# Performance work log

Hardware: AMD Instinct MI355X
Metric: run time of the kernel (lower is better)

The kernel has to match this reference:

```python
import jax, jax.numpy as jnp
import numpy as np

N, D_IN = 65536, 512
H1, H2, D_SH = 1024, 1024, 512   # shared net: num_nodes_shared = [1024, 1024, 512]
HI = 512                          # indiv hidden width, num_nodes_indiv = [512, 512]


def setup_inputs() -> dict:
    key = jax.random.key(0)
    ks = jax.random.split(key, 16)
    s = 0.02
    inp = {
        "input": jax.random.normal(ks[0], (N, D_IN), jnp.float32),
        "treatment": jax.random.randint(ks[1], (N,), 0, 2, jnp.int32),
        # shared net (hidden ReLU layers + linear output, all with bias)
        "W0": jax.random.normal(ks[2], (D_IN, H1), jnp.float32) * s,
        "b0": jnp.zeros((H1,), jnp.float32),
        "W1": jax.random.normal(ks[3], (H1, H2), jnp.float32) * s,
        "b1": jnp.zeros((H2,), jnp.float32),
        "W2": jax.random.normal(ks[4], (H2, D_SH), jnp.float32) * s,
        "b2": jnp.zeros((D_SH,), jnp.float32),
        # risk net 0 (output layer has no bias)
        "A0": jax.random.normal(ks[5], (D_SH, HI), jnp.float32) * s,
        "a0": jnp.zeros((HI,), jnp.float32),
        "A1": jax.random.normal(ks[6], (HI, HI), jnp.float32) * s,
        "a1": jnp.zeros((HI,), jnp.float32),
        "A2": jax.random.normal(ks[7], (HI, 1), jnp.float32) * s,
        # risk net 1
        "C0": jax.random.normal(ks[8], (D_SH, HI), jnp.float32) * s,
        "c0": jnp.zeros((HI,), jnp.float32),
        "C1": jax.random.normal(ks[9], (HI, HI), jnp.float32) * s,
        "c1": jnp.zeros((HI,), jnp.float32),
        "C2": jax.random.normal(ks[10], (HI, 1), jnp.float32) * s,
    }
    return inp


def _risk_net(h, U0, u0, U1, u1, U2):
    h = jax.nn.relu(h @ U0 + u0)
    h = jax.nn.relu(h @ U1 + u1)
    return h @ U2  # [N, 1], no output bias


def reference(input, treatment, W0, b0, W1, b1, W2, b2,
              A0, a0, A1, a1, A2, C0, c0, C1, c1, C2):
    # shared MLP
    h = jax.nn.relu(input @ W0 + b0)
    h = jax.nn.relu(h @ W1 + b1)
    out = h @ W2 + b2                     # [N, D_SH]
    # Binary expert routing. The torch code gathers samples per treatment,
    # runs each group through its own MLP and scatters results back; the
    # math is equivalent to applying both experts and selecting per sample.
    y0 = _risk_net(out, A0, a0, A1, a1, A2)[:, 0]  # [N]
    y1 = _risk_net(out, C0, c0, C1, c1, C2)[:, 0]  # [N]
    y = jnp.where(treatment == 0, y0, y1)          # [N]
    return (y, out)
```

## Files before the change

kernel.cpp:

```cpp
#include <hip/hip_runtime.h>
#include <hip/hip_bf16.h>
#include <stdint.h>

typedef short short8 __attribute__((ext_vector_type(8)));
typedef float f32x4 __attribute__((ext_vector_type(4)));

#define NSAMP 65536
#define AS1 __attribute__((address_space(1)))
#define AS3 __attribute__((address_space(3)))

__device__ __forceinline__ unsigned f2bf(float f) {
    union { float f; unsigned u; } v; v.f = f;
    unsigned u = v.u;
    u += 0x7fffu + ((u >> 16) & 1u);
    return u >> 16;
}


__global__ void k_convert_bf16(const float* __restrict__ in, unsigned short* __restrict__ out, int n8) {
    int i = blockIdx.x * blockDim.x + threadIdx.x;
    if (i >= n8) return;
    const float4* p = (const float4*)in + (size_t)i * 2;
    float4 a = p[0], b = p[1];
    short8 o;
    o[0] = (short)f2bf(a.x); o[1] = (short)f2bf(a.y);
    o[2] = (short)f2bf(a.z); o[3] = (short)f2bf(a.w);
    o[4] = (short)f2bf(b.x); o[5] = (short)f2bf(b.y);
    o[6] = (short)f2bf(b.z); o[7] = (short)f2bf(b.w);
    ((short8*)out)[i] = o;
}

struct PrepArgs {
    const float *W0, *W1, *W2, *A0, *C0, *A1, *C1, *a0v, *c0v;
    unsigned short *W0T, *W1T, *W2T, *RT0, *A1T, *C1T;
    float *bcat, *yout;
};
__global__ void k_prep(PrepArgs p) {
    int i = blockIdx.x * blockDim.x + threadIdx.x;
    if (i < 524288)  { int k = i >> 10, n = i & 1023; p.W0T[n * 512 + k] = f2bf(p.W0[i]); return; }
    i -= 524288;
    if (i < 1048576) { int k = i >> 10, n = i & 1023; p.W1T[n * 1024 + k] = f2bf(p.W1[i]); return; }
    i -= 1048576;
    if (i < 524288)  { int k = i >> 9, n = i & 511; p.W2T[n * 1024 + k] = f2bf(p.W2[i]); return; }
    i -= 524288;
    if (i < 262144)  { int k = i >> 9, n = i & 511; p.RT0[n * 512 + k] = f2bf(p.A0[i]); return; }
    i -= 262144;
    if (i < 262144)  { int k = i >> 9, n = i & 511; p.RT0[(512 + n) * 512 + k] = f2bf(p.C0[i]); return; }
    i -= 262144;
    if (i < 262144)  { int k = i >> 9, n = i & 511; p.A1T[n * 512 + k] = f2bf(p.A1[i]); return; }
    i -= 262144;
    if (i < 262144)  { int k = i >> 9, n = i & 511; p.C1T[n * 512 + k] = f2bf(p.C1[i]); return; }
    i -= 262144;
    if (i < 512)     { p.bcat[i] = p.a0v[i]; return; }
    i -= 512;
    if (i < 512)     { p.bcat[512 + i] = p.c0v[i]; return; }
    i -= 512;
    if (i < 65536)   { p.yout[i] = 0.f; return; }
}

template<int MODE>
__global__ __launch_bounds__(512, 2)
void k_gemm256(const unsigned short* __restrict__ A, int lda,
               const unsigned short* __restrict__ BT, const unsigned short* __restrict__ BT2,
               const float* __restrict__ bias, const float* __restrict__ bias2,
               unsigned short* __restrict__ Cbf, float* __restrict__ Cf32,
               const float* __restrict__ w2, const float* __restrict__ w2b,
               const int* __restrict__ TRt, float* __restrict__ ydot,
               int Ncols, int K, int TPB)
{
    __shared__ __align__(16) char lds[131072];

    const int tid  = threadIdx.x;
    const int lane = tid & 63;
    const int wid  = tid >> 6;
    const int wr   = wid >> 2;
    const int wcn  = wid & 3;

    const int bid = (int)((blockIdx.x & 7) * 32 + (blockIdx.x >> 3));
    const int cls = bid % TPB;
    const int w   = bid / TPB;
    const int MSTEP = 256 / TPB;

    int n0e, cOff = 0, expert = 0;
    const unsigned short* Bsel = BT;
    if (MODE == 2) {
        expert = cls >> 1;
        n0e = (cls & 1) << 8;
        cOff = expert << 9;
        if (expert) Bsel = BT2;
    } else {
        n0e = cls << 8;
    }

    const int srow = tid >> 2;
    const int scs  = (tid & 3) ^ ((srow >> 1) & 3);
    const int ldst = wid * 1024;

    const unsigned short* gB0 = Bsel + (size_t)(n0e + srow) * K + scs * 8;
    const unsigned short* gB1 = gB0 + (size_t)128 * K;
    const size_t dA = (size_t)MSTEP * 256 * lda;
    const unsigned short* cA0 = A + (size_t)((w << 8) + srow) * lda + cOff + scs * 8;
    const unsigned short* cA1 = cA0 + (size_t)128 * lda;

#define STAGE_BLK(dbuf, blkoff, g0, g1, koff)                                            \
    do {                                                                                 \
        __builtin_amdgcn_global_load_lds((const AS1 void*)((g0) + (koff)),               \
                                         (AS3 void*)((dbuf) + (blkoff) + ldst), 16, 0, 0); \
        __builtin_amdgcn_global_load_lds((const AS1 void*)((g1) + (koff)),               \
                                         (AS3 void*)((dbuf) + (blkoff) + 8192 + ldst), 16, 0, 0); \
    } while (0)

    int aOff[8], bOff[4];
#pragma unroll
    for (int i = 0; i < 8; ++i) {
        int r = wr * 128 + i * 16 + (lane & 15);
        aOff[i] = r * 64 + ((((lane >> 4) ^ ((r >> 1) & 3))) << 4);
    }
#pragma unroll
    for (int j = 0; j < 4; ++j) {
        int r = wcn * 64 + j * 16 + (lane & 15);
        bOff[j] = r * 64 + ((((lane >> 4) ^ ((r >> 1) & 3))) << 4);
    }

    f32x4 acc[8][4];
#pragma unroll
    for (int i = 0; i < 8; ++i)
#pragma unroll
        for (int j = 0; j < 4; ++j) acc[i][j] = (f32x4)0.f;

    const int KT  = K >> 6;
    const int TOT = TPB * KT;

    STAGE_BLK(lds, 0,     cA0, cA1, 0);
    STAGE_BLK(lds, 32768, gB0, gB1, 0);
    STAGE_BLK(lds, 16384, cA0, cA1, 32);
    STAGE_BLK(lds, 49152, gB0, gB1, 32);
    asm volatile("s_waitcnt vmcnt(4)" ::: "memory");
    __builtin_amdgcn_s_barrier();

    int g = 0;
    for (int tau = 0; tau < TPB; ++tau) {
        const unsigned short* nA0 = cA0 + dA;
        const unsigned short* nA1 = cA1 + dA;

        for (int t = 0; t < KT; ++t, ++g) {
            const char* sbuf = lds + (g & 1) * 65536;
            char* dbuf = lds + ((g + 1) & 1) * 65536;
            const bool inTile = (t + 1 < KT);
            const bool st = (g + 1 < TOT);
            const unsigned short* sA0 = inTile ? cA0 : nA0;
            const unsigned short* sA1 = inTile ? cA1 : nA1;
            const int koff = inTile ? ((t + 1) << 6) : 0;
            short8 af[4], bfv[4];

#pragma unroll
            for (int i = 0; i < 4; ++i) af[i]  = *(const short8*)(sbuf + aOff[i]);
#pragma unroll
            for (int j = 0; j < 4; ++j) bfv[j] = *(const short8*)(sbuf + 32768 + bOff[j]);
            if (st) STAGE_BLK(dbuf, 0, sA0, sA1, koff);
            __builtin_amdgcn_s_barrier();
            asm volatile("s_waitcnt lgkmcnt(0)" ::: "memory");
            __builtin_amdgcn_sched_barrier(0);
            __builtin_amdgcn_s_setprio(1);
#pragma unroll
            for (int i = 0; i < 4; ++i)
#pragma unroll
                for (int j = 0; j < 4; ++j)
                    acc[i][j] = __builtin_amdgcn_mfma_f32_16x16x32_bf16(bfv[j], af[i], acc[i][j], 0, 0, 0);
            __builtin_amdgcn_s_setprio(0);
            __builtin_amdgcn_s_barrier();

#pragma unroll
            for (int i = 0; i < 4; ++i) af[i] = *(const short8*)(sbuf + aOff[4 + i]);
            if (st) STAGE_BLK(dbuf, 32768, gB0, gB1, koff);
            __builtin_amdgcn_s_barrier();
            asm volatile("s_waitcnt lgkmcnt(0)" ::: "memory");
            __builtin_amdgcn_sched_barrier(0);
            __builtin_amdgcn_s_setprio(1);
#pragma unroll
            for (int i = 0; i < 4; ++i)
#pragma unroll
                for (int j = 0; j < 4; ++j)
                    acc[4 + i][j] = __builtin_amdgcn_mfma_f32_16x16x32_bf16(bfv[j], af[i], acc[4 + i][j], 0, 0, 0);
            __builtin_amdgcn_s_setprio(0);
            if (st) { asm volatile("s_waitcnt vmcnt(4)" ::: "memory"); }
            else    { asm volatile("s_waitcnt vmcnt(0)" ::: "memory"); }
            __builtin_amdgcn_sched_barrier(0);
            __builtin_amdgcn_s_barrier();

#pragma unroll
            for (int i = 0; i < 4; ++i) af[i]  = *(const short8*)(sbuf + 16384 + aOff[i]);
#pragma unroll
            for (int j = 0; j < 4; ++j) bfv[j] = *(const short8*)(sbuf + 49152 + bOff[j]);
            if (st) STAGE_BLK(dbuf, 16384, sA0, sA1, koff + 32);
            __builtin_amdgcn_s_barrier();
            asm volatile("s_waitcnt lgkmcnt(0)" ::: "memory");
            __builtin_amdgcn_sched_barrier(0);
            __builtin_amdgcn_s_setprio(1);
#pragma unroll
            for (int i = 0; i < 4; ++i)
#pragma unroll
                for (int j = 0; j < 4; ++j)
                    acc[i][j] = __builtin_amdgcn_mfma_f32_16x16x32_bf16(bfv[j], af[i], acc[i][j], 0, 0, 0);
            __builtin_amdgcn_s_setprio(0);
            __builtin_amdgcn_s_barrier();

#pragma unroll
            for (int i = 0; i < 4; ++i) af[i] = *(const short8*)(sbuf + 16384 + aOff[4 + i]);
            if (st) STAGE_BLK(dbuf, 49152, gB0, gB1, koff + 32);
            __builtin_amdgcn_s_barrier();
            asm volatile("s_waitcnt lgkmcnt(0)" ::: "memory");
            __builtin_amdgcn_sched_barrier(0);
            __builtin_amdgcn_s_setprio(1);
#pragma unroll
            for (int i = 0; i < 4; ++i)
#pragma unroll
                for (int j = 0; j < 4; ++j)
                    acc[4 + i][j] = __builtin_amdgcn_mfma_f32_16x16x32_bf16(bfv[j], af[i], acc[4 + i][j], 0, 0, 0);
            __builtin_amdgcn_s_setprio(0);
            if (st) { asm volatile("s_waitcnt vmcnt(4)" ::: "memory"); }
            __builtin_amdgcn_sched_barrier(0);
            __builtin_amdgcn_s_barrier();
        }

        const int m0 = (w + MSTEP * tau) << 8;
        if (MODE == 2) {
            const float* be = expert ? bias2 : bias;
            const float* we = expert ? w2b : w2;
            const int nb = n0e + wcn * 64 + ((lane >> 4) << 2);
            f32x4 bv[4], wv[4];
#pragma unroll
            for (int j = 0; j < 4; ++j) {
                bv[j] = *(const f32x4*)(be + nb + j * 16);
                wv[j] = *(const f32x4*)(we + nb + j * 16);
            }
#pragma unroll
            for (int i = 0; i < 8; ++i) {
                float p = 0.f;
#pragma unroll
                for (int j = 0; j < 4; ++j)
#pragma unroll
                    for (int r = 0; r < 4; ++r)
                        p += fmaxf(acc[i][j][r] + bv[j][r], 0.f) * wv[j][r];
                p += __shfl_xor(p, 16);
                p += __shfl_xor(p, 32);
                const int m = m0 + wr * 128 + i * 16 + (lane & 15);
                if (lane < 16 && TRt[m] == expert) atomicAdd(&ydot[m], p);
            }
        } else {
            const int nb = n0e + wcn * 64 + ((lane >> 4) << 2);
            f32x4 bv[4];
#pragma unroll
            for (int j = 0; j < 4; ++j) bv[j] = *(const f32x4*)(bias + nb + j * 16);
#pragma unroll
            for (int i = 0; i < 8; ++i) {
                const int m = m0 + wr * 128 + i * 16 + (lane & 15);
                unsigned short* pb = Cbf + (size_t)m * Ncols + nb;
#pragma unroll
                for (int j = 0; j < 4; ++j) {
                    f32x4 v = acc[i][j] + bv[j];
                    if (MODE == 0) {
#pragma unroll
                        for (int r = 0; r < 4; ++r) v[r] = fmaxf(v[r], 0.f);
                    }
                    if (MODE == 1) *(f32x4*)(Cf32 + (size_t)m * Ncols + nb + j * 16) = v;
                    unsigned long long pk =
                        (unsigned long long)(f2bf(v[0]) | (f2bf(v[1]) << 16)) |
                        ((unsigned long long)(f2bf(v[2]) | (f2bf(v[3]) << 16)) << 32);
                    *(unsigned long long*)(pb + j * 16) = pk;
                }
            }
        }

#pragma unroll
        for (int i = 0; i < 8; ++i)
#pragma unroll
            for (int j = 0; j < 4; ++j) acc[i][j] = (f32x4)0.f;
        cA0 = nA0; cA1 = nA1;
    }
#undef STAGE_BLK
}


extern "C" void kernel_launch(void* const* d_in, const int* in_sizes, int n_in,
                              void* d_out, int out_size, void* d_ws, size_t ws_size,
                              hipStream_t stream) {
    const float* X  = (const float*)d_in[0];
    const int*  TR  = (const int*)d_in[1];
    const float* W0 = (const float*)d_in[2];  const float* b0 = (const float*)d_in[3];
    const float* W1 = (const float*)d_in[4];  const float* b1 = (const float*)d_in[5];
    const float* W2 = (const float*)d_in[6];  const float* b2 = (const float*)d_in[7];
    const float* A0 = (const float*)d_in[8];  const float* a0 = (const float*)d_in[9];
    const float* A1 = (const float*)d_in[10]; const float* a1 = (const float*)d_in[11];
    const float* A2 = (const float*)d_in[12];
    const float* C0 = (const float*)d_in[13]; const float* c0 = (const float*)d_in[14];
    const float* C1 = (const float*)d_in[15]; const float* c1 = (const float*)d_in[16];
    const float* C2 = (const float*)d_in[17];

    float* y_out   = (float*)d_out;
    float* out_out = (float*)d_out + NSAMP;

    char* ws = (char*)d_ws;
    size_t off = 0;
    auto alloc = [&](size_t bytes) -> char* {
        char* p = ws + off;
        off += (bytes + 255) & ~(size_t)255;
        return p;
    };
    unsigned short* Xb  = (unsigned short*)alloc((size_t)NSAMP * 512 * 2);
    unsigned short* H1b = (unsigned short*)alloc((size_t)NSAMP * 1024 * 2);
    unsigned short* H2b = (unsigned short*)alloc((size_t)NSAMP * 1024 * 2);
    unsigned short* OUTb = H1b;
    unsigned short* R01  = H2b;
    unsigned short* W0T = (unsigned short*)alloc(512 * 1024 * 2);
    unsigned short* W1T = (unsigned short*)alloc(1024 * 1024 * 2);
    unsigned short* W2T = (unsigned short*)alloc(1024 * 512 * 2);
    unsigned short* RT0 = (unsigned short*)alloc(1024 * 512 * 2);
    unsigned short* A1T = (unsigned short*)alloc(512 * 512 * 2);
    unsigned short* C1T = (unsigned short*)alloc(512 * 512 * 2);
    float* bcat = (float*)alloc(1024 * 4);

    k_convert_bf16<<<(NSAMP * 512 / 8 + 255) / 256, 256, 0, stream>>>(X, Xb, NSAMP * 512 / 8);
    PrepArgs pa;
    pa.W0 = W0; pa.W1 = W1; pa.W2 = W2; pa.A0 = A0; pa.C0 = C0; pa.A1 = A1; pa.C1 = C1;
    pa.a0v = a0; pa.c0v = c0;
    pa.W0T = W0T; pa.W1T = W1T; pa.W2T = W2T; pa.RT0 = RT0; pa.A1T = A1T; pa.C1T = C1T;
    pa.bcat = bcat; pa.yout = y_out;
    k_prep<<<(3212288 + 255) / 256, 256, 0, stream>>>(pa);

    k_gemm256<0><<<256, 512, 0, stream>>>(Xb, 512, W0T, nullptr, b0, nullptr,
                                          H1b, nullptr, nullptr, nullptr, nullptr, nullptr,
                                          1024, 512, 4);
    k_gemm256<0><<<256, 512, 0, stream>>>(H1b, 1024, W1T, nullptr, b1, nullptr,
                                          H2b, nullptr, nullptr, nullptr, nullptr, nullptr,
                                          1024, 1024, 4);
    k_gemm256<1><<<256, 512, 0, stream>>>(H2b, 1024, W2T, nullptr, b2, nullptr,
                                          OUTb, out_out, nullptr, nullptr, nullptr, nullptr,
                                          512, 1024, 2);

    k_gemm256<0><<<256, 512, 0, stream>>>(OUTb, 512, RT0, nullptr, bcat, nullptr,
                                          R01, nullptr, nullptr, nullptr, nullptr, nullptr,
                                          1024, 512, 4);

    k_gemm256<2><<<256, 512, 0, stream>>>(R01, 1024, A1T, C1T, a1, c1,
                                          nullptr, nullptr, A2, C2, TR, y_out,
                                          512, 512, 4);
}
```

Before: 575.3 us.

## Prefetch LDS fragments across K-steps and cut per-step barriers in GEMM main loop

```diff
diff --git a/kernel.cpp b/kernel.cpp
--- a/kernel.cpp
+++ b/kernel.cpp
@@ -137,6 +137,13 @@
     STAGE_BLK(lds, 49152, gB0, gB1, 32);
     asm volatile("s_waitcnt vmcnt(4)" ::: "memory");
     __builtin_amdgcn_s_barrier();
+    __builtin_amdgcn_sched_barrier(0);
+
+    short8 pa[4], pb[4];
+#pragma unroll
+    for (int i = 0; i < 4; ++i) pa[i] = *(const short8*)(lds + aOff[i]);
+#pragma unroll
+    for (int j = 0; j < 4; ++j) pb[j] = *(const short8*)(lds + 32768 + bOff[j]);
 
     int g = 0;
     for (int tau = 0; tau < TPB; ++tau) {
@@ -151,76 +158,70 @@
             const unsigned short* sA0 = inTile ? cA0 : nA0;
             const unsigned short* sA1 = inTile ? cA1 : nA1;
             const int koff = inTile ? ((t + 1) << 6) : 0;
-            short8 af[4], bfv[4];
-
-#pragma unroll
-            for (int i = 0; i < 4; ++i) af[i]  = *(const short8*)(sbuf + aOff[i]);
-#pragma unroll
-            for (int j = 0; j < 4; ++j) bfv[j] = *(const short8*)(sbuf + 32768 + bOff[j]);
-            if (st) STAGE_BLK(dbuf, 0, sA0, sA1, koff);
-            __builtin_amdgcn_s_barrier();
-            asm volatile("s_waitcnt lgkmcnt(0)" ::: "memory");
-            __builtin_amdgcn_sched_barrier(0);
+            short8 xa[4];
+
+            if (st) {
+                STAGE_BLK(dbuf, 0,     sA0, sA1, koff);
+                STAGE_BLK(dbuf, 32768, gB0, gB1, koff);
+            }
+#pragma unroll
+            for (int i = 0; i < 4; ++i) xa[i] = *(const short8*)(sbuf + aOff[4 + i]);
             __builtin_amdgcn_s_setprio(1);
 #pragma unroll
             for (int i = 0; i < 4; ++i)
 #pragma unroll
                 for (int j = 0; j < 4; ++j)
-                    acc[i][j] = __builtin_amdgcn_mfma_f32_16x16x32_bf16(bfv[j], af[i], acc[i][j], 0, 0, 0);
+                    acc[i][j] = __builtin_amdgcn_mfma_f32_16x16x32_bf16(pb[j], pa[i], acc[i][j], 0, 0, 0);
             __builtin_amdgcn_s_setprio(0);
-            __builtin_amdgcn_s_barrier();
-
-#pragma unroll
-            for (int i = 0; i < 4; ++i) af[i] = *(const short8*)(sbuf + aOff[4 + i]);
-            if (st) STAGE_BLK(dbuf, 32768, gB0, gB1, koff);
-            __builtin_amdgcn_s_barrier();
-            asm volatile("s_waitcnt lgkmcnt(0)" ::: "memory");
-            __builtin_amdgcn_sched_barrier(0);
+
             __builtin_amdgcn_s_setprio(1);
 #pragma unroll
             for (int i = 0; i < 4; ++i)
 #pragma unroll
                 for (int j = 0; j < 4; ++j)
-                    acc[4 + i][j] = __builtin_amdgcn_mfma_f32_16x16x32_bf16(bfv[j], af[i], acc[4 + i][j], 0, 0, 0);
+                    acc[4 + i][j] = __builtin_amdgcn_mfma_f32_16x16x32_bf16(pb[j], xa[i], acc[4 + i][j], 0, 0, 0);
             __builtin_amdgcn_s_setprio(0);
             if (st) { asm volatile("s_waitcnt vmcnt(4)" ::: "memory"); }
             else    { asm volatile("s_waitcnt vmcnt(0)" ::: "memory"); }
             __builtin_amdgcn_sched_barrier(0);
             __builtin_amdgcn_s_barrier();
-
-#pragma unroll
-            for (int i = 0; i < 4; ++i) af[i]  = *(const short8*)(sbuf + 16384 + aOff[i]);
-#pragma unroll
-            for (int j = 0; j < 4; ++j) bfv[j] = *(const short8*)(sbuf + 49152 + bOff[j]);
-            if (st) STAGE_BLK(dbuf, 16384, sA0, sA1, koff + 32);
-            __builtin_amdgcn_s_barrier();
-            asm volatile("s_waitcnt lgkmcnt(0)" ::: "memory");
             __builtin_amdgcn_sched_barrier(0);
+
+#pragma unroll
+            for (int i = 0; i < 4; ++i) pa[i] = *(const short8*)(sbuf + 16384 + aOff[i]);
+#pragma unroll
+            for (int j = 0; j < 4; ++j) pb[j] = *(const short8*)(sbuf + 49152 + bOff[j]);
+            if (st) {
+                STAGE_BLK(dbuf, 16384, sA0, sA1, koff + 32);
+                STAGE_BLK(dbuf, 49152, gB0, gB1, koff + 32);
+            }
             __builtin_amdgcn_s_setprio(1);
 #pragma unroll
             for (int i = 0; i < 4; ++i)
 #pragma unroll
                 for (int j = 0; j < 4; ++j)
-                    acc[i][j] = __builtin_amdgcn_mfma_f32_16x16x32_bf16(bfv[j], af[i], acc[i][j], 0, 0, 0);
+                    acc[i][j] = __builtin_amdgcn_mfma_f32_16x16x32_bf16(pb[j], pa[i], acc[i][j], 0, 0, 0);
             __builtin_amdgcn_s_setprio(0);
-            __builtin_amdgcn_s_barrier();
-
-#pragma unroll
-            for (int i = 0; i < 4; ++i) af[i] = *(const short8*)(sbuf + 16384 + aOff[4 + i]);
-            if (st) STAGE_BLK(dbuf, 49152, gB0, gB1, koff + 32);
-            __builtin_amdgcn_s_barrier();
-            asm volatile("s_waitcnt lgkmcnt(0)" ::: "memory");
-            __builtin_amdgcn_sched_barrier(0);
+
+#pragma unroll
+            for (int i = 0; i < 4; ++i) xa[i] = *(const short8*)(sbuf + 16384 + aOff[4 + i]);
             __builtin_amdgcn_s_setprio(1);
 #pragma unroll
             for (int i = 0; i < 4; ++i)
 #pragma unroll
                 for (int j = 0; j < 4; ++j)
-                    acc[4 + i][j] = __builtin_amdgcn_mfma_f32_16x16x32_bf16(bfv[j], af[i], acc[4 + i][j], 0, 0, 0);
+                    acc[4 + i][j] = __builtin_amdgcn_mfma_f32_16x16x32_bf16(pb[j], xa[i], acc[4 + i][j], 0, 0, 0);
             __builtin_amdgcn_s_setprio(0);
-            if (st) { asm volatile("s_waitcnt vmcnt(4)" ::: "memory"); }
-            __builtin_amdgcn_sched_barrier(0);
-            __builtin_amdgcn_s_barrier();
+            if (st) {
+                asm volatile("s_waitcnt vmcnt(4)" ::: "memory");
+                __builtin_amdgcn_sched_barrier(0);
+                __builtin_amdgcn_s_barrier();
+                __builtin_amdgcn_sched_barrier(0);
+#pragma unroll
+                for (int i = 0; i < 4; ++i) pa[i] = *(const short8*)(dbuf + aOff[i]);
+#pragma unroll
+                for (int j = 0; j < 4; ++j) pb[j] = *(const short8*)(dbuf + 32768 + bOff[j]);
+            }
         }
 
         const int m0 = (w + MSTEP * tau) << 8;
@@ -255,7 +256,7 @@
 #pragma unroll
             for (int i = 0; i < 8; ++i) {
                 const int m = m0 + wr * 128 + i * 16 + (lane & 15);
-                unsigned short* pb = Cbf + (size_t)m * Ncols + nb;
+                unsigned short* pbc = Cbf + (size_t)m * Ncols + nb;
 #pragma unroll
                 for (int j = 0; j < 4; ++j) {
                     f32x4 v = acc[i][j] + bv[j];
@@ -267,7 +268,7 @@
                     unsigned long long pk =
                         (unsigned long long)(f2bf(v[0]) | (f2bf(v[1]) << 16)) |
                         ((unsigned long long)(f2bf(v[2]) | (f2bf(v[3]) << 16)) << 32);
-                    *(unsigned long long*)(pb + j * 16) = pk;
+                    *(unsigned long long*)(pbc + j * 16) = pk;
                 }
             }
         }
```

Measured after the change: 573.0 us. No clear change (-0.4%).
